# Performance work log

Hardware: AMD Instinct MI355X
Metric: run time of the kernel (lower is better)

Reference implementation:

```python
import jax, jax.numpy as jnp
import numpy as np

N, F, E, C, CELL = 2048, 64, 4, 3, 15
OUT_CH, OUT_K, N_CLASS = 10, 15, 2


def _xex(X, A_attr, wx0, wx1, we):
    # pairwise score tensor: Y[i,j] = X[i]@wx0 + X[j]@wx1 + A_attr[i,j]@we -> [N,N,c_out]
    return (X @ wx0)[:, None, :] + (X @ wx1)[None, :, :] + jnp.einsum('ije,ec->ijc', A_attr, we)


def _gcn_layer(X, A, A_attr, ax0, ax1, ae, ix0, ix1, ie, gx0, gx1, ge, wr):
    n = X.shape[0]
    # multi-channel attention (MA) branch
    att = jax.nn.elu(_xex(X, A_attr, ax0, ax1, ae)) + 1.0001  # [n,n,C]
    att = att * A[:, :, None]
    att = jax.nn.softmax(att, axis=1)  # softmax over neighbor axis (incl. zeroed entries, as in TF code)
    att = att * A[:, :, None]
    y_node = jnp.einsum('ijc,jf->icf', att, X).reshape(n, -1)        # [n, C*F_in]
    y_edge = jnp.einsum('ijc,ije->ice', att, A_attr).reshape(n, -1)  # [n, C*E]
    # gated branch (unmasked sum over all j, as in aggr_neibors_gate)
    info = jnp.tanh(_xex(X, A_attr, ix0, ix1, ie))        # [n,n,CELL]
    gate = jax.nn.sigmoid(_xex(X, A_attr, gx0, gx1, ge))  # [n,n,CELL]
    y_gate = jnp.sum(info * gate, axis=1)                 # [n, CELL]
    r = jnp.concatenate([X, y_edge, y_node, y_gate], axis=1)
    return jnp.tanh(r @ wr + 0.1)


def _forward(X, A, A_attr,
             att0_x0, att0_x1, att0_e, info0_x0, info0_x1, info0_e,
             gate0_x0, gate0_x1, gate0_e, r0,
             att1_x0, att1_x1, att1_e, info1_x0, info1_x1, info1_e,
             gate1_x0, gate1_x1, gate1_e, r1,
             out_att, out_cnn, out_r):
    h0 = _gcn_layer(X, A, A_attr, att0_x0, att0_x1, att0_e,
                    info0_x0, info0_x1, info0_e, gate0_x0, gate0_x1, gate0_e, r0)
    h1 = _gcn_layer(h0, A, A_attr, att1_x0, att1_x1, att1_e,
                    info1_x0, info1_x1, info1_e, gate1_x0, gate1_x1, gate1_e, r1)
    Xc = jnp.concatenate([X, h0, h1], axis=1)       # [n, F + 2*CELL]
    att = jax.nn.softmax(Xc @ out_att, axis=0)      # node-wise attention pooling, [n, OUT_CH]
    image = att.T @ Xc                              # [OUT_CH, F + 2*CELL]
    image = jnp.tanh(image @ out_cnn + 0.1)         # [OUT_CH, OUT_K]
    logits = image.reshape(1, -1) @ out_r + 0.1
    return jax.nn.softmax(logits, axis=-1)          # [1, N_CLASS]


def setup_inputs() -> dict:
    keys = jax.random.split(jax.random.key(0), 26)
    tn = lambda k, s: jax.random.normal(k, s, jnp.float32) * 0.05  # truncated_normal init approx
    return {
        'X': jax.random.normal(keys[0], (N, F), jnp.float32),
        'A': (jax.random.uniform(keys[1], (N, N)) < 0.02).astype(jnp.float32),  # ~40 neighbors/node
        'A_attr': jax.random.normal(keys[2], (N, N, E), jnp.float32),
        'att0_x0': tn(keys[3], (F, C)), 'att0_x1': tn(keys[4], (F, C)), 'att0_e': tn(keys[5], (E, C)),
        'info0_x0': tn(keys[6], (F, CELL)), 'info0_x1': tn(keys[7], (F, CELL)), 'info0_e': tn(keys[8], (E, CELL)),
        'gate0_x0': tn(keys[9], (F, CELL)), 'gate0_x1': tn(keys[10], (F, CELL)), 'gate0_e': tn(keys[11], (E, CELL)),
        'r0': tn(keys[12], (F + (F + E) * C + CELL, CELL)),
        'att1_x0': tn(keys[13], (CELL, C)), 'att1_x1': tn(keys[14], (CELL, C)), 'att1_e': tn(keys[15], (E, C)),
        'info1_x0': tn(keys[16], (CELL, CELL)), 'info1_x1': tn(keys[17], (CELL, CELL)), 'info1_e': tn(keys[18], (E, CELL)),
        'gate1_x0': tn(keys[19], (CELL, CELL)), 'gate1_x1': tn(keys[20], (CELL, CELL)), 'gate1_e': tn(keys[21], (E, CELL)),
        'r1': tn(keys[22], (CELL + (CELL + E) * C + CELL, CELL)),
        'out_att': tn(keys[23], (F + 2 * CELL, OUT_CH)),
        'out_cnn': tn(keys[24], (F + 2 * CELL, OUT_K)),
        'out_r': tn(keys[25], (OUT_K * OUT_CH, N_CLASS)),
    }


def reference(X, A, A_attr,
              att0_x0, att0_x1, att0_e, info0_x0, info0_x1, info0_e,
              gate0_x0, gate0_x1, gate0_e, r0,
              att1_x0, att1_x1, att1_e, info1_x0, info1_x1, info1_e,
              gate1_x0, gate1_x1, gate1_e, r1,
              out_att, out_cnn, out_r):
    return _forward(X, A, A_attr,
                    att0_x0, att0_x1, att0_e, info0_x0, info0_x1, info0_e,
                    gate0_x0, gate0_x1, gate0_e, r0,
                    att1_x0, att1_x1, att1_e, info1_x0, info1_x1, info1_e,
                    gate1_x0, gate1_x1, gate1_e, r1,
                    out_att, out_cnn, out_r)
```

## Files before the change

kernel.cpp:

```cpp
#include <hip/hip_runtime.h>
#include <hip/hip_bf16.h>
#include <math.h>

#define NN 2048
#define EE 4
#define CC 3
#define CELL 15
#define MAXD 128
#define GATE_JZ 4

typedef unsigned short u16;
typedef float f32x2 __attribute__((ext_vector_type(2)));

__device__ __forceinline__ float b2f(u16 u) { return __uint_as_float(((unsigned int)u) << 16); }
__device__ __forceinline__ u16 f2b(float f) {
    unsigned int x = __float_as_uint(f);
    unsigned int r = (x + 0x7fffu + ((x >> 16) & 1u)) >> 16;
    return (u16)r;
}
__device__ __forceinline__ float fastrcp(float x) { return __builtin_amdgcn_rcpf(x); }
__device__ __forceinline__ float fastexp2(float x) { return __builtin_amdgcn_exp2f(x); }
__device__ __forceinline__ float rfl(float x) {
    return __uint_as_float(__builtin_amdgcn_readfirstlane(__float_as_uint(x)));
}
__device__ __forceinline__ float ldx(const void* p, size_t i, bool bf) {
    if (bf) return b2f(((const u16*)p)[i]);
    return ((const float*)p)[i];
}
__device__ __forceinline__ bool detect_bf(const u16* X) {
    int lane = threadIdx.x & 63;
    u16 u = X[2 * lane];
    int e = (u >> 7) & 0xFF;
    unsigned long long m = __ballot(e >= 100 && e <= 150);
    return __popcll(m) >= 32;
}

__global__ __launch_bounds__(256) void k_edges(const void* __restrict__ A, const u16* __restrict__ Xd,
                                               int* __restrict__ flag, int* __restrict__ deg,
                                               int* __restrict__ edges, float* __restrict__ imgp) {
    bool bf = detect_bf(Xd);
    if (blockIdx.x == 0) {
        if (threadIdx.x == 0) *flag = bf ? 1 : 0;
        for (int q = threadIdx.x; q < 940; q += 256) imgp[q] = 0.f;
    }
    int lane = threadIdx.x & 63, wv = threadIdx.x >> 6;
    int i = blockIdx.x * 4 + wv;
    int base = 0;
    for (int jb = 0; jb < NN; jb += 64) {
        float a = ldx(A, (size_t)i * NN + jb + lane, bf);
        unsigned long long m = __ballot(a != 0.f);
        if (a != 0.f) {
            int slot = base + __popcll(m & ((1ull << lane) - 1ull));
            if (slot < MAXD) edges[i * MAXD + slot] = jb + lane;
        }
        base += __popcll(m);
    }
    if (lane == 0) deg[i] = base;
}

template<int FIN, bool XRAW>
__global__ void k_proj(const int* __restrict__ flag, const void* __restrict__ Xin_,
                       const void* __restrict__ ax0, const void* __restrict__ ax1,
                       const void* __restrict__ ix0, const void* __restrict__ ix1,
                       const void* __restrict__ gx0, const void* __restrict__ gx1,
                       float* __restrict__ p0, float* __restrict__ pj,
                       float* __restrict__ pa0, float* __restrict__ pa1) {
    __shared__ float xs[FIN];
    bool bf = (*flag != 0);
    bool xbf = XRAW ? bf : false;
    int nd = blockIdx.x;
    int t = threadIdx.x;
    if (t < FIN) xs[t] = ldx(Xin_, (size_t)nd * FIN + t, xbf);
    __syncthreads();
    if (t >= 66) return;
    const void* W; int col, OUT; float* dst;
    if (t < 15)      { W = ix0; col = t;      OUT = CELL; dst = p0  + nd * 30 + t; }
    else if (t < 30) { W = gx0; col = t - 15; OUT = CELL; dst = p0  + nd * 30 + t; }
    else if (t < 45) { W = ix1; col = t - 30; OUT = CELL; dst = pj  + nd * 30 + (t - 30); }
    else if (t < 60) { W = gx1; col = t - 45; OUT = CELL; dst = pj  + nd * 30 + (t - 30); }
    else if (t < 63) { W = ax0; col = t - 60; OUT = CC;   dst = pa0 + nd * 3 + (t - 60); }
    else             { W = ax1; col = t - 63; OUT = CC;   dst = pa1 + nd * 3 + (t - 63); }
    float acc = 0.f;
    for (int f = 0; f < FIN; ++f) acc += xs[f] * ldx(W, (size_t)f * OUT + col, bf);
    *dst = acc;
}

template<int FIN, bool BF, bool XRAW>
__device__ void att_body(const void* __restrict__ Xin_, const void* __restrict__ A_attr,
                         const void* __restrict__ ae,
                         const float* __restrict__ pa0, const float* __restrict__ pa1,
                         const int* __restrict__ deg, const int* __restrict__ edges,
                         float* __restrict__ y_node, float* __restrict__ y_edge,
                         float (*ew)[4], float* pdn, float* pne, float* pnn) {
    int i = blockIdx.x;
    int t = threadIdx.x;
    int lane = t & 63, wv = t >> 6;
    float aew[EE][CC];
    #pragma unroll
    for (int e = 0; e < EE; ++e)
        #pragma unroll
        for (int c = 0; c < CC; ++c) aew[e][c] = ldx(ae, e * CC + c, BF);
    float pa0v[3] = { pa0[i*3], pa0[i*3+1], pa0[i*3+2] };
    int dg = deg[i]; if (dg > MAXD) dg = MAXD;
    float dn[3] = {0.f, 0.f, 0.f};
    float ne[3][4] = {{0.f}};
    for (int base = 0; base < dg; base += 256) {
        int idx = base + t;
        if (idx < dg) {
            int j = edges[i * MAXD + idx];
            float a0, a1, a2, a3;
            if (BF) {
                const u16* ap = (const u16*)A_attr + ((size_t)i * NN + j) * EE;
                ushort4 av = *(const ushort4*)ap;
                a0 = b2f(av.x); a1 = b2f(av.y); a2 = b2f(av.z); a3 = b2f(av.w);
            } else {
                const float* ap = (const float*)A_attr + ((size_t)i * NN + j) * EE;
                float4 av = *(const float4*)ap;
                a0 = av.x; a1 = av.y; a2 = av.z; a3 = av.w;
            }
            float w[3];
            #pragma unroll
            for (int c = 0; c < 3; ++c) {
                float s = pa0v[c] + pa1[j*3 + c]
                        + a0*aew[0][c] + a1*aew[1][c] + a2*aew[2][c] + a3*aew[3][c];
                float val = (s > 0.f) ? (s + 1.0001f) : (__expf(s) - 1.f + 1.0001f);
                float wc = __expf(val);
                w[c] = wc;
                dn[c] += wc;
                ne[c][0] += wc * a0; ne[c][1] += wc * a1; ne[c][2] += wc * a2; ne[c][3] += wc * a3;
            }
            ew[idx][0] = __int_as_float(j);
            ew[idx][1] = w[0]; ew[idx][2] = w[1]; ew[idx][3] = w[2];
        }
    }
    #pragma unroll
    for (int off = 32; off; off >>= 1) {
        #pragma unroll
        for (int c = 0; c < 3; ++c) {
            dn[c] += __shfl_xor(dn[c], off);
            #pragma unroll
            for (int e = 0; e < 4; ++e) ne[c][e] += __shfl_xor(ne[c][e], off);
        }
    }
    if (lane == 0) {
        #pragma unroll
        for (int c = 0; c < 3; ++c) {
            pdn[wv*3 + c] = dn[c];
            #pragma unroll
            for (int e = 0; e < 4; ++e) pne[(wv*3 + c)*4 + e] = ne[c][e];
        }
    }
    __syncthreads();
    float rdn[3];
    #pragma unroll
    for (int c = 0; c < 3; ++c) {
        float s = (float)(NN - dg);
        #pragma unroll
        for (int w2 = 0; w2 < 4; ++w2) s += pdn[w2*3 + c];
        rdn[c] = 1.f / s;
    }
    float nn0 = 0.f, nn1 = 0.f, nn2 = 0.f;
    bool xbf = XRAW ? BF : false;
    if constexpr (FIN == 15) {
        int sub = lane >> 4, f = lane & 15;
        for (int idx = wv * 4 + sub; idx < dg; idx += 16) {
            int j = __float_as_int(ew[idx][0]);
            float w0 = ew[idx][1], w1 = ew[idx][2], w2 = ew[idx][3];
            if (f < 15) {
                float x = ldx(Xin_, (size_t)j * 15 + f, xbf);
                nn0 += w0 * x; nn1 += w1 * x; nn2 += w2 * x;
            }
        }
        pnn[(wv*3 + 0)*64 + lane] = nn0;
        pnn[(wv*3 + 1)*64 + lane] = nn1;
        pnn[(wv*3 + 2)*64 + lane] = nn2;
    } else {
        for (int idx = wv; idx < dg; idx += 4) {
            int j = __float_as_int(ew[idx][0]);
            float w0 = ew[idx][1], w1 = ew[idx][2], w2 = ew[idx][3];
            if (lane < FIN) {
                float x = ldx(Xin_, (size_t)j * FIN + lane, xbf);
                nn0 += w0 * x; nn1 += w1 * x; nn2 += w2 * x;
            }
        }
        if (lane < FIN) {
            pnn[(wv*3 + 0)*64 + lane] = nn0;
            pnn[(wv*3 + 1)*64 + lane] = nn1;
            pnn[(wv*3 + 2)*64 + lane] = nn2;
        }
    }
    __syncthreads();
    if constexpr (FIN == 15) {
        if (t < 15) {
            #pragma unroll
            for (int c = 0; c < 3; ++c) {
                float s = 0.f;
                #pragma unroll
                for (int w2 = 0; w2 < 4; ++w2)
                    #pragma unroll
                    for (int sb = 0; sb < 4; ++sb)
                        s += pnn[(w2*3 + c)*64 + sb*16 + t];
                y_node[(size_t)i * 45 + c*15 + t] = s * rdn[c];
            }
        }
    } else {
        if (t < FIN) {
            #pragma unroll
            for (int c = 0; c < 3; ++c) {
                float s = pnn[(0*3+c)*64 + t] + pnn[(1*3+c)*64 + t]
                        + pnn[(2*3+c)*64 + t] + pnn[(3*3+c)*64 + t];
                y_node[(size_t)i * (3*FIN) + c*FIN + t] = s * rdn[c];
            }
        }
    }
    if (t == 0) {
        #pragma unroll
        for (int c = 0; c < 3; ++c)
            #pragma unroll
            for (int e = 0; e < 4; ++e) {
                float s = pne[(0*3+c)*4+e] + pne[(1*3+c)*4+e] + pne[(2*3+c)*4+e] + pne[(3*3+c)*4+e];
                y_edge[(size_t)i * 12 + c*4 + e] = s * rdn[c];
            }
    }
}

template<int FIN, bool XRAW>
__global__ __launch_bounds__(256) void k_att(
        const int* __restrict__ flag,
        const void* __restrict__ Xin_, const void* __restrict__ A_attr, const void* __restrict__ ae,
        const float* __restrict__ pa0, const float* __restrict__ pa1,
        const int* __restrict__ deg, const int* __restrict__ edges,
        float* __restrict__ y_node, float* __restrict__ y_edge) {
    __shared__ float ew[MAXD][4];
    __shared__ float pdn[4*3];
    __shared__ float pne[4*3*4];
    __shared__ float pnn[4*3*64];
    if (*flag) att_body<FIN, true,  XRAW>(Xin_, A_attr, ae, pa0, pa1, deg, edges, y_node, y_edge, ew, pdn, pne, pnn);
    else       att_body<FIN, false, XRAW>(Xin_, A_attr, ae, pa0, pa1, deg, edges, y_node, y_edge, ew, pdn, pne, pnn);
}

template<bool BF, int K0, int NK>
__device__ void gate_body(const void* __restrict__ A_attr,
                          const void* __restrict__ iew, const void* __restrict__ gew,
                          const float* __restrict__ p0, const float* __restrict__ pj,
                          float* __restrict__ ygp, float* lds) {
    constexpr int JCH = NN / GATE_JZ;
    constexpr float L2E = 1.4426950408889634f;
    const int lane = threadIdx.x & 63;
    const int wv = threadIdx.x >> 6;
    const int i = blockIdx.x * 8 + wv;
    const int jb0 = blockIdx.z * JCH;

    {
        int r = threadIdx.x;
        const float* src = pj + (size_t)(jb0 + r) * 30;
        float* dst = lds + r * 18;
        #pragma unroll
        for (int k = 0; k < NK; ++k) {
            dst[2*k]     = src[K0 + k]      * (-2.f * L2E);
            dst[2*k + 1] = src[15 + K0 + k] * (-L2E);
        }
    }
    f32x2 W2[EE][NK];
    #pragma unroll
    for (int e = 0; e < EE; ++e)
        #pragma unroll
        for (int k = 0; k < NK; ++k) {
            W2[e][k].x = rfl(ldx(iew, e*CELL + K0 + k, BF) * (-2.f * L2E));
            W2[e][k].y = rfl(ldx(gew, e*CELL + K0 + k, BF) * (-L2E));
        }
    f32x2 p0p[NK];
    #pragma unroll
    for (int k = 0; k < NK; ++k) {
        p0p[k].x = rfl(p0[(size_t)i*30 + K0 + k] * (-2.f * L2E));
        p0p[k].y = rfl(p0[(size_t)i*30 + 15 + K0 + k] * (-L2E));
    }
    __syncthreads();

    float acc[NK] = {0.f};
    #pragma unroll 2
    for (int jg = 0; jg < JCH; jg += 64) {
        int r = jg + lane;
        int j = jb0 + r;
        float a0, a1, a2, a3;
        if (BF) {
            const u16* ap = (const u16*)A_attr + ((size_t)i * NN + j) * EE;
            ushort4 av = *(const ushort4*)ap;
            a0 = b2f(av.x); a1 = b2f(av.y); a2 = b2f(av.z); a3 = b2f(av.w);
        } else {
            const float* ap = (const float*)A_attr + ((size_t)i * NN + j) * EE;
            float4 av = *(const float4*)ap;
            a0 = av.x; a1 = av.y; a2 = av.z; a3 = av.w;
        }
        f32x2 aa0 = {a0, a0}, aa1 = {a1, a1}, aa2 = {a2, a2}, aa3 = {a3, a3};
        const float* rowp = lds + r * 18;
        #pragma unroll
        for (int k = 0; k < NK; ++k) {
            f32x2 tu = *(const f32x2*)(rowp + 2*k) + p0p[k];
            tu += aa0 * W2[0][k];
            tu += aa1 * W2[1][k];
            tu += aa2 * W2[2][k];
            tu += aa3 * W2[3][k];
            float e1 = fastexp2(tu.x);
            float e2 = fastexp2(tu.y);
            float d1 = 1.f + e1, d2 = 1.f + e2;
            acc[k] = fmaf(1.f - e1, fastrcp(d1 * d2), acc[k]);
        }
    }
    #pragma unroll
    for (int off = 32; off; off >>= 1)
        #pragma unroll
        for (int k = 0; k < NK; ++k) acc[k] += __shfl_xor(acc[k], off);
    if (lane == 0) {
        #pragma unroll
        for (int k = 0; k < NK; ++k)
            ygp[((size_t)blockIdx.z * NN + i) * CELL + K0 + k] = acc[k];
    }
}

__global__ __launch_bounds__(512, 4) void k_gate(
        const int* __restrict__ flag,
        const void* __restrict__ A_attr, const void* __restrict__ iew, const void* __restrict__ gew,
        const float* __restrict__ p0, const float* __restrict__ pj, float* __restrict__ ygp) {
    __shared__ __align__(16) float lds[512 * 18];
    if (*flag) {
        if (blockIdx.y == 0) gate_body<true, 0, 8>(A_attr, iew, gew, p0, pj, ygp, lds);
        else                 gate_body<true, 8, 7>(A_attr, iew, gew, p0, pj, ygp, lds);
    } else {
        if (blockIdx.y == 0) gate_body<false, 0, 8>(A_attr, iew, gew, p0, pj, ygp, lds);
        else                 gate_body<false, 8, 7>(A_attr, iew, gew, p0, pj, ygp, lds);
    }
}

__global__ __launch_bounds__(256) void k_hp(const int* __restrict__ flag,
        const void* __restrict__ X, const float* __restrict__ y_edge,
        const float* __restrict__ y_node, const float* __restrict__ y_gate,
        const void* __restrict__ wr,
        const void* __restrict__ ax0, const void* __restrict__ ax1,
        const void* __restrict__ ix0, const void* __restrict__ ix1,
        const void* __restrict__ gx0, const void* __restrict__ gx1,
        float* __restrict__ h0,
        float* __restrict__ p0o, float* __restrict__ pjo,
        float* __restrict__ pa0o, float* __restrict__ pa1o) {
    __shared__ float v[283];
    __shared__ float part[CELL][16];
    __shared__ float hs[CELL];
    bool bf = (*flag != 0);
    int nd = blockIdx.x, t = threadIdx.x;
    for (int q = t; q < 64; q += 256)  v[q]       = ldx(X, (size_t)nd * 64 + q, bf);
    for (int q = t; q < 12; q += 256)  v[64 + q]  = y_edge[(size_t)nd * 12 + q];
    for (int q = t; q < 192; q += 256) v[76 + q]  = y_node[(size_t)nd * 192 + q];
    for (int q = t; q < 15; q += 256) {
        float s = 0.f;
        #pragma unroll
        for (int z = 0; z < GATE_JZ; ++z) s += y_gate[((size_t)z * NN + nd) * CELL + q];
        v[268 + q] = s;
    }
    __syncthreads();
    if (t < 240) {
        int k = t >> 4, sub = t & 15;
        float acc = 0.f;
        for (int r = sub; r < 283; r += 16) acc += v[r] * ldx(wr, (size_t)r * CELL + k, bf);
        part[k][sub] = acc;
    }
    __syncthreads();
    if (t < CELL) {
        float acc = 0.1f;
        #pragma unroll
        for (int s = 0; s < 16; ++s) acc += part[t][s];
        float hv = tanhf(acc);
        hs[t] = hv;
        h0[(size_t)nd * CELL + t] = hv;
    }
    __syncthreads();
    if (t < 66) {
        const void* W; int col, OUT; float* dst;
        if (t < 15)      { W = ix0; col = t;      OUT = CELL; dst = p0o  + nd * 30 + t; }
        else if (t < 30) { W = gx0; col = t - 15; OUT = CELL; dst = p0o  + nd * 30 + t; }
        else if (t < 45) { W = ix1; col = t - 30; OUT = CELL; dst = pjo  + nd * 30 + (t - 30); }
        else if (t < 60) { W = gx1; col = t - 45; OUT = CELL; dst = pjo  + nd * 30 + (t - 30); }
        else if (t < 63) { W = ax0; col = t - 60; OUT = CC;   dst = pa0o + nd * 3 + (t - 60); }
        else             { W = ax1; col = t - 63; OUT = CC;   dst = pa1o + nd * 3 + (t - 63); }
        float acc = 0.f;
        for (int f = 0; f < CELL; ++f) acc += hs[f] * ldx(W, (size_t)f * OUT + col, bf);
        *dst = acc;
    }
}

__global__ __launch_bounds__(256) void k_hf(const int* __restrict__ flag,
        const void* __restrict__ X, const float* __restrict__ h0,
        const float* __restrict__ y_edge, const float* __restrict__ y_node,
        const float* __restrict__ y_gate, const void* __restrict__ wr,
        const void* __restrict__ oatt,
        float* __restrict__ h1, float* __restrict__ P) {
    __shared__ float v[87];
    __shared__ float xv[64];
    __shared__ float part[CELL][16];
    __shared__ float hs[CELL];
    __shared__ float pp[10][16];
    bool bf = (*flag != 0);
    int nd = blockIdx.x, t = threadIdx.x;
    for (int q = t; q < 15; q += 256) v[q]      = h0[(size_t)nd * 15 + q];
    for (int q = t; q < 12; q += 256) v[15 + q] = y_edge[(size_t)nd * 12 + q];
    for (int q = t; q < 45; q += 256) v[27 + q] = y_node[(size_t)nd * 45 + q];
    for (int q = t; q < 15; q += 256) {
        float s = 0.f;
        #pragma unroll
        for (int z = 0; z < GATE_JZ; ++z) s += y_gate[((size_t)z * NN + nd) * CELL + q];
        v[72 + q] = s;
    }
    for (int q = t; q < 64; q += 256) xv[q]     = ldx(X, (size_t)nd * 64 + q, bf);
    __syncthreads();
    if (t < 240) {
        int k = t >> 4, sub = t & 15;
        float acc = 0.f;
        for (int r = sub; r < 87; r += 16) acc += v[r] * ldx(wr, (size_t)r * CELL + k, bf);
        part[k][sub] = acc;
    }
    __syncthreads();
    if (t < CELL) {
        float acc = 0.1f;
        #pragma unroll
        for (int s = 0; s < 16; ++s) acc += part[t][s];
        float hv = tanhf(acc);
        hs[t] = hv;
        h1[(size_t)nd * CELL + t] = hv;
    }
    __syncthreads();
    if (t < 160) {
        int c = t >> 4, sub = t & 15;
        float acc = 0.f;
        for (int d = sub; d < 94; d += 16) {
            float x = (d < 64) ? xv[d] : (d < 79) ? v[d - 64] : hs[d - 79];
            acc += x * ldx(oatt, (size_t)d * 10 + c, bf);
        }
        pp[c][sub] = acc;
    }
    __syncthreads();
    if (t < 10) {
        float acc = 0.f;
        #pragma unroll
        for (int s = 0; s < 16; ++s) acc += pp[t][s];
        P[(size_t)nd * 10 + t] = acc;
    }
}

__global__ __launch_bounds__(1024) void k_f3(const int* __restrict__ flag,
                     const void* __restrict__ X, const float* __restrict__ h0,
                     const float* __restrict__ h1, const float* __restrict__ P,
                     float* __restrict__ image_pre) {
    __shared__ float red[16][10];
    __shared__ float wsl[32][10];
    bool bf = (*flag != 0);
    int t = threadIdx.x; int lane = t & 63; int wv = t >> 6;
    float mx[10], sm[10];
    #pragma unroll
    for (int c = 0; c < 10; ++c) mx[c] = -1e30f;
    for (int n = t; n < NN; n += 1024)
        #pragma unroll
        for (int c = 0; c < 10; ++c) mx[c] = fmaxf(mx[c], P[(size_t)n*10 + c]);
    #pragma unroll
    for (int off = 32; off; off >>= 1)
        #pragma unroll
        for (int c = 0; c < 10; ++c) mx[c] = fmaxf(mx[c], __shfl_xor(mx[c], off));
    if (lane == 0)
        #pragma unroll
        for (int c = 0; c < 10; ++c) red[wv][c] = mx[c];
    __syncthreads();
    #pragma unroll
    for (int c = 0; c < 10; ++c) {
        float m = red[0][c];
        for (int w2 = 1; w2 < 16; ++w2) m = fmaxf(m, red[w2][c]);
        mx[c] = m;
    }
    __syncthreads();
    #pragma unroll
    for (int c = 0; c < 10; ++c) sm[c] = 0.f;
    for (int n = t; n < NN; n += 1024)
        #pragma unroll
        for (int c = 0; c < 10; ++c) sm[c] += __expf(P[(size_t)n*10 + c] - mx[c]);
    #pragma unroll
    for (int off = 32; off; off >>= 1)
        #pragma unroll
        for (int c = 0; c < 10; ++c) sm[c] += __shfl_xor(sm[c], off);
    if (lane == 0)
        #pragma unroll
        for (int c = 0; c < 10; ++c) red[wv][c] = sm[c];
    __syncthreads();
    float rs[10];
    #pragma unroll
    for (int c = 0; c < 10; ++c) {
        float s = 0.f;
        for (int w2 = 0; w2 < 16; ++w2) s += red[w2][c];
        rs[c] = 1.f / s;
    }
    int n0 = blockIdx.x * 32;
    if (t < 320) {
        int nl = t / 10, c = t - nl * 10;
        wsl[nl][c] = __expf(P[(size_t)(n0 + nl)*10 + c] - mx[c]) * rs[c];
    }
    __syncthreads();
    if (t < 940) {
        int ch = t / 94, d = t - ch * 94;
        float acc = 0.f;
        for (int nl = 0; nl < 32; ++nl) {
            int n = n0 + nl;
            float w = wsl[nl][ch];
            float x = (d < 64) ? ldx(X, (size_t)n*64 + d, bf)
                    : (d < 79) ? h0[(size_t)n*15 + (d - 64)]
                               : h1[(size_t)n*15 + (d - 79)];
            acc += w * x;
        }
        atomicAdd(&image_pre[t], acc);
    }
}

__global__ __launch_bounds__(256) void k_f4(const int* __restrict__ flag,
                     const float* __restrict__ image_pre,
                     const void* __restrict__ out_cnn, const void* __restrict__ out_r,
                     void* __restrict__ out) {
    bool bf = (*flag != 0);
    __shared__ float ip[940];
    __shared__ float img2[150];
    __shared__ float red[8];
    int t = threadIdx.x;
    for (int q = t; q < 940; q += 256) ip[q] = image_pre[q];
    __syncthreads();
    if (t < 150) {
        int ch = t / 15, kk = t - ch * 15;
        float acc = 0.1f;
        for (int d = 0; d < 94; ++d) acc += ip[ch*94 + d] * ldx(out_cnn, (size_t)d*15 + kk, bf);
        img2[t] = tanhf(acc);
    }
    __syncthreads();
    float c0 = 0.f, c1 = 0.f;
    if (t < 150) {
        float vv = img2[t];
        c0 = vv * ldx(out_r, (size_t)t*2, bf);
        c1 = vv * ldx(out_r, (size_t)t*2 + 1, bf);
    }
    #pragma unroll
    for (int off = 32; off; off >>= 1) { c0 += __shfl_xor(c0, off); c1 += __shfl_xor(c1, off); }
    if ((t & 63) == 0) { red[(t >> 6)*2] = c0; red[(t >> 6)*2 + 1] = c1; }
    __syncthreads();
    if (t == 0) {
        float l0 = 0.1f + red[0] + red[2] + red[4] + red[6];
        float l1 = 0.1f + red[1] + red[3] + red[5] + red[7];
        float m = fmaxf(l0, l1);
        float e0 = __expf(l0 - m), e1 = __expf(l1 - m);
        float s = e0 + e1;
        float p0v = e0 / s, p1v = e1 / s;
        if (bf) { u16* o = (u16*)out; o[0] = f2b(p0v); o[1] = f2b(p1v); }
        else    { float* o = (float*)out; o[0] = p0v; o[1] = p1v; }
    }
}

extern "C" void kernel_launch(void* const* d_in, const int* in_sizes, int n_in,
                              void* d_out, int out_size, void* d_ws, size_t ws_size,
                              hipStream_t stream) {
    (void)in_sizes; (void)n_in; (void)out_size; (void)ws_size;
    const void* X      = d_in[0];
    const void* A      = d_in[1];
    const void* Aattr  = d_in[2];
    const void* a0x0 = d_in[3],  *a0x1 = d_in[4],  *a0e = d_in[5];
    const void* i0x0 = d_in[6],  *i0x1 = d_in[7],  *i0e = d_in[8];
    const void* g0x0 = d_in[9],  *g0x1 = d_in[10], *g0e = d_in[11];
    const void* r0   = d_in[12];
    const void* a1x0 = d_in[13], *a1x1 = d_in[14], *a1e = d_in[15];
    const void* i1x0 = d_in[16], *i1x1 = d_in[17], *i1e = d_in[18];
    const void* g1x0 = d_in[19], *g1x1 = d_in[20], *g1e = d_in[21];
    const void* r1   = d_in[22];
    const void* oatt = d_in[23], *ocnn = d_in[24], *orr = d_in[25];

    char* p = (char*)d_ws;
    auto alloc = [&](size_t bytes) -> void* { void* r = (void*)p; p += (bytes + 255) & ~(size_t)255; return r; };
    int*   flag   = (int*)  alloc(4);
    int*   deg    = (int*)  alloc(NN * 4);
    int*   edges  = (int*)  alloc((size_t)NN * MAXD * 4);
    float* p0_0   = (float*)alloc((size_t)NN * 30 * 4);
    float* pj_0   = (float*)alloc((size_t)NN * 30 * 4);
    float* pa0_0  = (float*)alloc((size_t)NN * 3 * 4);
    float* pa1_0  = (float*)alloc((size_t)NN * 3 * 4);
    float* p0_1   = (float*)alloc((size_t)NN * 30 * 4);
    float* pj_1   = (float*)alloc((size_t)NN * 30 * 4);
    float* pa0_1  = (float*)alloc((size_t)NN * 3 * 4);
    float* pa1_1  = (float*)alloc((size_t)NN * 3 * 4);
    float* ye0    = (float*)alloc((size_t)NN * 12 * 4);
    float* yn0    = (float*)alloc((size_t)NN * 192 * 4);
    float* yg0    = (float*)alloc((size_t)GATE_JZ * NN * CELL * 4);
    float* h0     = (float*)alloc((size_t)NN * CELL * 4);
    float* ye1    = (float*)alloc((size_t)NN * 12 * 4);
    float* yn1    = (float*)alloc((size_t)NN * 45 * 4);
    float* yg1    = (float*)alloc((size_t)GATE_JZ * NN * CELL * 4);
    float* h1     = (float*)alloc((size_t)NN * CELL * 4);
    float* P      = (float*)alloc((size_t)NN * 10 * 4);
    float* imgp   = (float*)alloc(940 * 4);

    k_edges<<<NN / 4, 256, 0, stream>>>(A, (const u16*)X, flag, deg, edges, imgp);

    dim3 ggate(NN / 8, 2, GATE_JZ);

    k_proj<64, true><<<NN, 128, 0, stream>>>(flag, X, a0x0, a0x1, i0x0, i0x1, g0x0, g0x1, p0_0, pj_0, pa0_0, pa1_0);
    k_att<64, true><<<NN, 256, 0, stream>>>(flag, X, Aattr, a0e, pa0_0, pa1_0, deg, edges, yn0, ye0);
    k_gate<<<ggate, 512, 0, stream>>>(flag, Aattr, i0e, g0e, p0_0, pj_0, yg0);
    k_hp<<<NN, 256, 0, stream>>>(flag, X, ye0, yn0, yg0, r0,
                                 a1x0, a1x1, i1x0, i1x1, g1x0, g1x1,
                                 h0, p0_1, pj_1, pa0_1, pa1_1);

    k_att<15, false><<<NN, 256, 0, stream>>>(flag, h0, Aattr, a1e, pa0_1, pa1_1, deg, edges, yn1, ye1);
    k_gate<<<ggate, 512, 0, stream>>>(flag, Aattr, i1e, g1e, p0_1, pj_1, yg1);
    k_hf<<<NN, 256, 0, stream>>>(flag, X, h0, ye1, yn1, yg1, r1, oatt, h1, P);

    k_f3<<<64, 1024, 0, stream>>>(flag, X, h0, h1, P, imgp);
    k_f4<<<1, 256, 0, stream>>>(flag, imgp, ocnn, orr, d_out);
}
```

Before: 340.0 us.

## Fuse layer-0 projection into edge kernel and phase gate LDS staging

Merges the first-layer node projection into the edge-list kernel as extra blocks, each handling two nodes, which removes a separate launch. The gate kernel now stages the projected neighbor terms into shared memory in 256-row phases rather than all 512 at once, halving LDS per block. This is meant to cut launch overhead and could raise occupancy, but it adds barriers inside the gate loop.

```diff
diff --git a/kernel.cpp b/kernel.cpp
--- a/kernel.cpp
+++ b/kernel.cpp
@@ -37,52 +37,52 @@
 
 __global__ __launch_bounds__(256) void k_edges(const void* __restrict__ A, const u16* __restrict__ Xd,
                                                int* __restrict__ flag, int* __restrict__ deg,
-                                               int* __restrict__ edges, float* __restrict__ imgp) {
+                                               int* __restrict__ edges, float* __restrict__ imgp,
+                                               const void* __restrict__ X,
+                                               const void* __restrict__ ax0, const void* __restrict__ ax1,
+                                               const void* __restrict__ ix0, const void* __restrict__ ix1,
+                                               const void* __restrict__ gx0, const void* __restrict__ gx1,
+                                               float* __restrict__ p0, float* __restrict__ pj,
+                                               float* __restrict__ pa0, float* __restrict__ pa1) {
+    __shared__ float xs[2][64];
     bool bf = detect_bf(Xd);
-    if (blockIdx.x == 0) {
-        if (threadIdx.x == 0) *flag = bf ? 1 : 0;
-        for (int q = threadIdx.x; q < 940; q += 256) imgp[q] = 0.f;
-    }
-    int lane = threadIdx.x & 63, wv = threadIdx.x >> 6;
-    int i = blockIdx.x * 4 + wv;
-    int base = 0;
-    for (int jb = 0; jb < NN; jb += 64) {
-        float a = ldx(A, (size_t)i * NN + jb + lane, bf);
-        unsigned long long m = __ballot(a != 0.f);
-        if (a != 0.f) {
-            int slot = base + __popcll(m & ((1ull << lane) - 1ull));
-            if (slot < MAXD) edges[i * MAXD + slot] = jb + lane;
-        }
-        base += __popcll(m);
-    }
-    if (lane == 0) deg[i] = base;
-}
-
-template<int FIN, bool XRAW>
-__global__ void k_proj(const int* __restrict__ flag, const void* __restrict__ Xin_,
-                       const void* __restrict__ ax0, const void* __restrict__ ax1,
-                       const void* __restrict__ ix0, const void* __restrict__ ix1,
-                       const void* __restrict__ gx0, const void* __restrict__ gx1,
-                       float* __restrict__ p0, float* __restrict__ pj,
-                       float* __restrict__ pa0, float* __restrict__ pa1) {
-    __shared__ float xs[FIN];
-    bool bf = (*flag != 0);
-    bool xbf = XRAW ? bf : false;
-    int nd = blockIdx.x;
-    int t = threadIdx.x;
-    if (t < FIN) xs[t] = ldx(Xin_, (size_t)nd * FIN + t, xbf);
-    __syncthreads();
-    if (t >= 66) return;
-    const void* W; int col, OUT; float* dst;
-    if (t < 15)      { W = ix0; col = t;      OUT = CELL; dst = p0  + nd * 30 + t; }
-    else if (t < 30) { W = gx0; col = t - 15; OUT = CELL; dst = p0  + nd * 30 + t; }
-    else if (t < 45) { W = ix1; col = t - 30; OUT = CELL; dst = pj  + nd * 30 + (t - 30); }
-    else if (t < 60) { W = gx1; col = t - 45; OUT = CELL; dst = pj  + nd * 30 + (t - 30); }
-    else if (t < 63) { W = ax0; col = t - 60; OUT = CC;   dst = pa0 + nd * 3 + (t - 60); }
-    else             { W = ax1; col = t - 63; OUT = CC;   dst = pa1 + nd * 3 + (t - 63); }
-    float acc = 0.f;
-    for (int f = 0; f < FIN; ++f) acc += xs[f] * ldx(W, (size_t)f * OUT + col, bf);
-    *dst = acc;
+    if (blockIdx.x < NN / 4) {
+        if (blockIdx.x == 0) {
+            if (threadIdx.x == 0) *flag = bf ? 1 : 0;
+            for (int q = threadIdx.x; q < 940; q += 256) imgp[q] = 0.f;
+        }
+        int lane = threadIdx.x & 63, wv = threadIdx.x >> 6;
+        int i = blockIdx.x * 4 + wv;
+        int base = 0;
+        for (int jb = 0; jb < NN; jb += 64) {
+            float a = ldx(A, (size_t)i * NN + jb + lane, bf);
+            unsigned long long m = __ballot(a != 0.f);
+            if (a != 0.f) {
+                int slot = base + __popcll(m & ((1ull << lane) - 1ull));
+                if (slot < MAXD) edges[i * MAXD + slot] = jb + lane;
+            }
+            base += __popcll(m);
+        }
+        if (lane == 0) deg[i] = base;
+    } else {
+        int nb = blockIdx.x - NN / 4;
+        int sel = threadIdx.x >> 7;
+        int tl = threadIdx.x & 127;
+        int nd = nb * 2 + sel;
+        if (tl < 64) xs[sel][tl] = ldx(X, (size_t)nd * 64 + tl, bf);
+        __syncthreads();
+        if (tl >= 66) return;
+        const void* W; int col, OUT; float* dst;
+        if (tl < 15)      { W = ix0; col = tl;      OUT = CELL; dst = p0  + nd * 30 + tl; }
+        else if (tl < 30) { W = gx0; col = tl - 15; OUT = CELL; dst = p0  + nd * 30 + tl; }
+        else if (tl < 45) { W = ix1; col = tl - 30; OUT = CELL; dst = pj  + nd * 30 + (tl - 30); }
+        else if (tl < 60) { W = gx1; col = tl - 45; OUT = CELL; dst = pj  + nd * 30 + (tl - 30); }
+        else if (tl < 63) { W = ax0; col = tl - 60; OUT = CC;   dst = pa0 + nd * 3 + (tl - 60); }
+        else              { W = ax1; col = tl - 63; OUT = CC;   dst = pa1 + nd * 3 + (tl - 63); }
+        float acc = 0.f;
+        for (int f = 0; f < 64; ++f) acc += xs[sel][f] * ldx(W, (size_t)f * OUT + col, bf);
+        *dst = acc;
+    }
 }
 
 template<int FIN, bool BF, bool XRAW>
@@ -245,22 +245,13 @@
                           const float* __restrict__ p0, const float* __restrict__ pj,
                           float* __restrict__ ygp, float* lds) {
     constexpr int JCH = NN / GATE_JZ;
+    constexpr int PH = 256;
     constexpr float L2E = 1.4426950408889634f;
     const int lane = threadIdx.x & 63;
     const int wv = threadIdx.x >> 6;
     const int i = blockIdx.x * 8 + wv;
     const int jb0 = blockIdx.z * JCH;
 
-    {
-        int r = threadIdx.x;
-        const float* src = pj + (size_t)(jb0 + r) * 30;
-        float* dst = lds + r * 18;
-        #pragma unroll
-        for (int k = 0; k < NK; ++k) {
-            dst[2*k]     = src[K0 + k]      * (-2.f * L2E);
-            dst[2*k + 1] = src[15 + K0 + k] * (-L2E);
-        }
-    }
     f32x2 W2[EE][NK];
     #pragma unroll
     for (int e = 0; e < EE; ++e)
@@ -275,36 +266,51 @@
         p0p[k].x = rfl(p0[(size_t)i*30 + K0 + k] * (-2.f * L2E));
         p0p[k].y = rfl(p0[(size_t)i*30 + 15 + K0 + k] * (-L2E));
     }
-    __syncthreads();
 
     float acc[NK] = {0.f};
-    #pragma unroll 2
-    for (int jg = 0; jg < JCH; jg += 64) {
-        int r = jg + lane;
-        int j = jb0 + r;
-        float a0, a1, a2, a3;
-        if (BF) {
-            const u16* ap = (const u16*)A_attr + ((size_t)i * NN + j) * EE;
-            ushort4 av = *(const ushort4*)ap;
-            a0 = b2f(av.x); a1 = b2f(av.y); a2 = b2f(av.z); a3 = b2f(av.w);
-        } else {
-            const float* ap = (const float*)A_attr + ((size_t)i * NN + j) * EE;
-            float4 av = *(const float4*)ap;
-            a0 = av.x; a1 = av.y; a2 = av.z; a3 = av.w;
-        }
-        f32x2 aa0 = {a0, a0}, aa1 = {a1, a1}, aa2 = {a2, a2}, aa3 = {a3, a3};
-        const float* rowp = lds + r * 18;
-        #pragma unroll
-        for (int k = 0; k < NK; ++k) {
-            f32x2 tu = *(const f32x2*)(rowp + 2*k) + p0p[k];
-            tu += aa0 * W2[0][k];
-            tu += aa1 * W2[1][k];
-            tu += aa2 * W2[2][k];
-            tu += aa3 * W2[3][k];
-            float e1 = fastexp2(tu.x);
-            float e2 = fastexp2(tu.y);
-            float d1 = 1.f + e1, d2 = 1.f + e2;
-            acc[k] = fmaf(1.f - e1, fastrcp(d1 * d2), acc[k]);
+    for (int ph = 0; ph < JCH; ph += PH) {
+        if (ph) __syncthreads();
+        {
+            int r = threadIdx.x;
+            if (r < PH) {
+                const float* src = pj + (size_t)(jb0 + ph + r) * 30;
+                float* dst = lds + r * 18;
+                #pragma unroll
+                for (int k = 0; k < NK; ++k) {
+                    dst[2*k]     = src[K0 + k]      * (-2.f * L2E);
+                    dst[2*k + 1] = src[15 + K0 + k] * (-L2E);
+                }
+            }
+        }
+        __syncthreads();
+        #pragma unroll 2
+        for (int jgl = 0; jgl < PH; jgl += 64) {
+            int lr = jgl + lane;
+            int j = jb0 + ph + lr;
+            float a0, a1, a2, a3;
+            if (BF) {
+                const u16* ap = (const u16*)A_attr + ((size_t)i * NN + j) * EE;
+                ushort4 av = *(const ushort4*)ap;
+                a0 = b2f(av.x); a1 = b2f(av.y); a2 = b2f(av.z); a3 = b2f(av.w);
+            } else {
+                const float* ap = (const float*)A_attr + ((size_t)i * NN + j) * EE;
+                float4 av = *(const float4*)ap;
+                a0 = av.x; a1 = av.y; a2 = av.z; a3 = av.w;
+            }
+            f32x2 aa0 = {a0, a0}, aa1 = {a1, a1}, aa2 = {a2, a2}, aa3 = {a3, a3};
+            const float* rowp = lds + lr * 18;
+            #pragma unroll
+            for (int k = 0; k < NK; ++k) {
+                f32x2 tu = *(const f32x2*)(rowp + 2*k) + p0p[k];
+                tu += aa0 * W2[0][k];
+                tu += aa1 * W2[1][k];
+                tu += aa2 * W2[2][k];
+                tu += aa3 * W2[3][k];
+                float e1 = fastexp2(tu.x);
+                float e2 = fastexp2(tu.y);
+                float d1 = 1.f + e1, d2 = 1.f + e2;
+                acc[k] = fmaf(1.f - e1, fastrcp(d1 * d2), acc[k]);
+            }
         }
     }
     #pragma unroll
@@ -322,7 +328,7 @@
         const int* __restrict__ flag,
         const void* __restrict__ A_attr, const void* __restrict__ iew, const void* __restrict__ gew,
         const float* __restrict__ p0, const float* __restrict__ pj, float* __restrict__ ygp) {
-    __shared__ __align__(16) float lds[512 * 18];
+    __shared__ __align__(16) float lds[256 * 18];
     if (*flag) {
         if (blockIdx.y == 0) gate_body<true, 0, 8>(A_attr, iew, gew, p0, pj, ygp, lds);
         else                 gate_body<true, 8, 7>(A_attr, iew, gew, p0, pj, ygp, lds);
@@ -596,11 +602,12 @@
     float* P      = (float*)alloc((size_t)NN * 10 * 4);
     float* imgp   = (float*)alloc(940 * 4);
 
-    k_edges<<<NN / 4, 256, 0, stream>>>(A, (const u16*)X, flag, deg, edges, imgp);
+    k_edges<<<NN / 4 + NN / 2, 256, 0, stream>>>(A, (const u16*)X, flag, deg, edges, imgp,
+                                                 X, a0x0, a0x1, i0x0, i0x1, g0x0, g0x1,
+                                                 p0_0, pj_0, pa0_0, pa1_0);
 
     dim3 ggate(NN / 8, 2, GATE_JZ);
 
-    k_proj<64, true><<<NN, 128, 0, stream>>>(flag, X, a0x0, a0x1, i0x0, i0x1, g0x0, g0x1, p0_0, pj_0, pa0_0, pa1_0);
     k_att<64, true><<<NN, 256, 0, stream>>>(flag, X, Aattr, a0e, pa0_0, pa1_0, deg, edges, yn0, ye0);
     k_gate<<<ggate, 512, 0, stream>>>(flag, Aattr, i0e, g0e, p0_0, pj_0, yg0);
     k_hp<<<NN, 256, 0, stream>>>(flag, X, ye0, yn0, yg0, r0,
```

Result: no change. 335.2 us (-1.4%).
